# Optimization experiments

Measured on AMD Instinct MI355X. Metric: run time of the kernel, lower is better.

The kernel has to match this reference:

```python
import jax, jax.numpy as jnp
import numpy as np

VOCAB, DIM = 50257, 128
B, R, C, T = 8, 100, 100, 20


def setup_inputs() -> dict:
    key = jax.random.key(0)
    k1, k2, k3 = jax.random.split(key, 3)
    x = jax.random.randint(k1, (B, R, C, T), 0, VOCAB, dtype=jnp.int32)
    emb = jax.random.normal(k2, (VOCAB, DIM), dtype=jnp.float32)
    W = jax.random.normal(k3, (DIM, 1), dtype=jnp.float32) / np.sqrt(DIM)
    b = jnp.zeros((1,), dtype=jnp.float32)
    return {"x": x, "emb": emb, "W": W, "b": b}


def reference(x, emb, W, b):
    # x: [B,R,C,T] int ids -> gather: [B,R,C,T,D]
    e = emb[x]
    # aggregate = mean over tokens (dropout is identity in eval)
    agg = e.mean(axis=-2)                      # [B,R,C,D]
    h = jax.nn.gelu(agg, approximate=False)    # exact erf GELU (torch default)
    logits = jnp.einsum('brcd,do->brc', h, W) + b[0]
    return logits                              # [B,R,C]
```

## Files before the change

### kernel.cpp

```cpp
#include <hip/hip_runtime.h>
#include <hip/hip_bf16.h>
#include <math.h>

constexpr int T_TOK  = 20;
constexpr int DIM    = 128;
constexpr int VOCAB  = 50257;
constexpr int NSLICE = 4;
constexpr int SDIM   = DIM / NSLICE;

typedef unsigned int  uint32x4 __attribute__((ext_vector_type(4)));
typedef float         f32x2    __attribute__((ext_vector_type(2)));

__device__ __forceinline__ float erf_fast(float z) {
    const float az = fabsf(z);
    const float t  = __builtin_amdgcn_rcpf(fmaf(0.3275911f, az, 1.0f));
    float poly = fmaf(fmaf(fmaf(fmaf(1.061405429f, t, -1.453152027f),
                                t, 1.421413741f),
                           t, -0.284496736f),
                      t, 0.254829592f);
    poly *= t;
    const float e = __expf(-az * az);
    const float r = fmaf(-poly, e, 1.0f);
    return copysignf(r, z);
}

__global__ __launch_bounds__(256) void convert_kernel(
    const float* __restrict__ emb, const float* __restrict__ b,
    ushort* __restrict__ embt, float* __restrict__ out,
    int nb_emb, int n_out)
{
    if ((int)blockIdx.x < nb_emb) {
        const int i = blockIdx.x * 256 + threadIdx.x;
        if (i >= VOCAB * (DIM / 8)) return;
        const int v  = i >> 4;
        const int jc = i & 15;
        const int s  = jc >> 2;
        const int jj = jc & 3;

        const float* src = emb + (size_t)v * DIM + jc * 8;
        const float4 a = *reinterpret_cast<const float4*>(src);
        const float4 c = *reinterpret_cast<const float4*>(src + 4);

        auto pack2 = [](float lo, float hi) -> unsigned int {
            unsigned int l = __bfloat16_as_ushort(__float2bfloat16(lo));
            unsigned int h = __bfloat16_as_ushort(__float2bfloat16(hi));
            return l | (h << 16);
        };
        uint32x4 u = { pack2(a.x, a.y), pack2(a.z, a.w), pack2(c.x, c.y), pack2(c.z, c.w) };
        *reinterpret_cast<uint32x4*>(embt + ((size_t)s * VOCAB + v) * SDIM + jj * 8) = u;
    } else {
        const int i = ((int)blockIdx.x - nb_emb) * 256 + threadIdx.x;
        if (i < n_out) out[i] = b[0];
    }
}

__global__ __launch_bounds__(256) void gather_kernel(
    const int* __restrict__ x,
    const ushort* __restrict__ embt,
    const float* __restrict__ W,
    float* __restrict__ out,
    int n_out)
{
    const int s = blockIdx.x & (NSLICE - 1);
    const int o = ((int)blockIdx.x >> 2) * 32 + ((int)threadIdx.x >> 3);
    const int h = ((int)threadIdx.x >> 2) & 1;
    const int j = threadIdx.x & 3;
    if (o >= n_out) return;

    const int* xo = x + (size_t)o * T_TOK;
    int ids[10];
    {
        const int4 a = *reinterpret_cast<const int4*>(xo + (h ? 12 : 0));
        const int4 c = *reinterpret_cast<const int4*>(xo + (h ? 16 : 4));
        const int2 e = *reinterpret_cast<const int2*>(xo + (h ? 10 : 8));
        ids[0] = a.x; ids[1] = a.y; ids[2] = a.z; ids[3] = a.w;
        ids[4] = c.x; ids[5] = c.y; ids[6] = c.z; ids[7] = c.w;
        ids[8] = e.x; ids[9] = e.y;
    }

    const ushort* base = embt + (size_t)s * VOCAB * SDIM + j * 8;
    f32x2 acc[4] = {{0.f,0.f},{0.f,0.f},{0.f,0.f},{0.f,0.f}};

    #pragma unroll
    for (int t = 0; t < 10; ++t) {
        const uint32x4 u = *reinterpret_cast<const uint32x4*>(base + (size_t)ids[t] * SDIM);
        #pragma unroll
        for (int q = 0; q < 4; ++q) {
            f32x2 v = { __uint_as_float(u[q] << 16), __uint_as_float(u[q] & 0xffff0000u) };
            acc[q] += v;
        }
    }

    const float lo[4] = { acc[0].x, acc[0].y, acc[1].x, acc[1].y };
    const float hi[4] = { acc[2].x, acc[2].y, acc[3].x, acc[3].y };
    float sum[4];
    #pragma unroll
    for (int k = 0; k < 4; ++k) {
        const float send = (h == 0) ? hi[k] : lo[k];
        const float recv = __shfl_xor(send, 4, 64);
        const float keep = (h == 0) ? lo[k] : hi[k];
        sum[k] = keep + recv;
    }

    const float c_z = (1.0f / (float)T_TOK) * 0.70710678118654752440f;
    const float c_h = 0.5f / (float)T_TOK;
    const float* wp = W + s * SDIM + j * 8 + h * 4;
    float p = 0.f;
    #pragma unroll
    for (int k = 0; k < 4; ++k) {
        const float w  = wp[k];
        const float t1 = sum[k] * c_h * w;
        const float r  = erf_fast(sum[k] * c_z);
        p = fmaf(t1, r, p + t1);
    }

    p += __shfl_xor(p, 1, 64);
    p += __shfl_xor(p, 2, 64);
    p += __shfl_xor(p, 4, 64);

    if ((threadIdx.x & 7) == 0)
        __hip_atomic_fetch_add(out + o, p, __ATOMIC_RELAXED, __HIP_MEMORY_SCOPE_AGENT);
}

__global__ __launch_bounds__(256) void gelu_embed_fallback(
    const int* __restrict__ x, const float* __restrict__ emb,
    const float* __restrict__ W, const float* __restrict__ b,
    float* __restrict__ out, int n_out)
{
    const int wave = (int)((blockIdx.x * blockDim.x + threadIdx.x) >> 6);
    const int lane = (int)(threadIdx.x & 63);
    if (wave >= n_out) return;
    const int* ids = x + (size_t)wave * T_TOK;
    float2 acc = make_float2(0.f, 0.f);
    #pragma unroll
    for (int t = 0; t < T_TOK; ++t) {
        const int id = ids[t];
        const float2 v = *reinterpret_cast<const float2*>(
            emb + (size_t)id * DIM + (size_t)(lane * 2));
        acc.x += v.x; acc.y += v.y;
    }
    const float inv_t = 1.0f / (float)T_TOK;
    const float ax = acc.x * inv_t, ay = acc.y * inv_t;
    const float kInvSqrt2 = 0.70710678118654752440f;
    const float gx = 0.5f * ax * (1.0f + erff(ax * kInvSqrt2));
    const float gy = 0.5f * ay * (1.0f + erff(ay * kInvSqrt2));
    const float2 w = *reinterpret_cast<const float2*>(W + (size_t)(lane * 2));
    float p = gx * w.x + gy * w.y;
    #pragma unroll
    for (int off = 32; off >= 1; off >>= 1) p += __shfl_down(p, off, 64);
    if (lane == 0) out[wave] = p + b[0];
}

extern "C" void kernel_launch(void* const* d_in, const int* in_sizes, int n_in,
                              void* d_out, int out_size, void* d_ws, size_t ws_size,
                              hipStream_t stream) {
    const int*   x   = (const int*)d_in[0];
    const float* emb = (const float*)d_in[1];
    const float* W   = (const float*)d_in[2];
    const float* b   = (const float*)d_in[3];
    float* out = (float*)d_out;
    const int n_out = out_size;

    const size_t embt_bytes = (size_t)NSLICE * VOCAB * SDIM * sizeof(ushort);

    if (ws_size < embt_bytes) {
        const int blocks = (n_out + 3) / 4;
        gelu_embed_fallback<<<blocks, 256, 0, stream>>>(x, emb, W, b, out, n_out);
        return;
    }

    ushort* embt = (ushort*)d_ws;

    {
        const int nb_emb = (VOCAB * (DIM / 8) + 255) / 256;
        const int nb_out = (n_out + 255) / 256;
        convert_kernel<<<nb_emb + nb_out, 256, 0, stream>>>(emb, b, embt, out,
                                                            nb_emb, n_out);
    }
    {
        const int nchunk = (n_out + 31) / 32;
        gather_kernel<<<NSLICE * nchunk, 256, 0, stream>>>(x, embt, W, out, n_out);
    }
}
```

Baseline: 46.10 us.

## Assign embedding slices to blocks by XCC id via atomic work tickets

```diff
diff --git a/kernel.cpp b/kernel.cpp
--- a/kernel.cpp
+++ b/kernel.cpp
@@ -7,6 +7,7 @@
 constexpr int VOCAB  = 50257;
 constexpr int NSLICE = 4;
 constexpr int SDIM   = DIM / NSLICE;
+constexpr int OUTS_PER_BLOCK = 32;
 
 typedef unsigned int  uint32x4 __attribute__((ext_vector_type(4)));
 typedef float         f32x2    __attribute__((ext_vector_type(2)));
@@ -26,7 +27,7 @@
 
 __global__ __launch_bounds__(256) void convert_kernel(
     const float* __restrict__ emb, const float* __restrict__ b,
-    ushort* __restrict__ embt, float* __restrict__ out,
+    ushort* __restrict__ embt, float* __restrict__ out, int* __restrict__ ctr,
     int nb_emb, int n_out)
 {
     if ((int)blockIdx.x < nb_emb) {
@@ -51,6 +52,7 @@
     } else {
         const int i = ((int)blockIdx.x - nb_emb) * 256 + threadIdx.x;
         if (i < n_out) out[i] = b[0];
+        if (i < NSLICE) ctr[i] = 0;
     }
 }
 
@@ -59,10 +61,28 @@
     const ushort* __restrict__ embt,
     const float* __restrict__ W,
     float* __restrict__ out,
-    int n_out)
+    int* __restrict__ ctr,
+    int n_out, int nchunk)
 {
-    const int s = blockIdx.x & (NSLICE - 1);
-    const int o = ((int)blockIdx.x >> 2) * 32 + ((int)threadIdx.x >> 3);
+    __shared__ int s_ticket[2];
+    if (threadIdx.x == 0) {
+        const unsigned xcc = __builtin_amdgcn_s_getreg(((4 - 1) << 11) | 20);
+        const int pref = (int)(xcc & 3u);
+        int ss = -1, cc = -1;
+        for (int q = 0; q < NSLICE; ++q) {
+            const int s2 = (pref + q) & (NSLICE - 1);
+            const int t  = __hip_atomic_fetch_add(&ctr[s2], 1,
+                             __ATOMIC_RELAXED, __HIP_MEMORY_SCOPE_AGENT);
+            if (t < nchunk) { ss = s2; cc = t; break; }
+        }
+        s_ticket[0] = ss; s_ticket[1] = cc;
+    }
+    __syncthreads();
+    const int s = s_ticket[0];
+    const int c = s_ticket[1];
+    if (s < 0) return;
+
+    const int o = c * OUTS_PER_BLOCK + ((int)threadIdx.x >> 3);
     const int h = ((int)threadIdx.x >> 2) & 1;
     const int j = threadIdx.x & 3;
     if (o >= n_out) return;
@@ -71,10 +91,10 @@
     int ids[10];
     {
         const int4 a = *reinterpret_cast<const int4*>(xo + (h ? 12 : 0));
-        const int4 c = *reinterpret_cast<const int4*>(xo + (h ? 16 : 4));
+        const int4 cc4 = *reinterpret_cast<const int4*>(xo + (h ? 16 : 4));
         const int2 e = *reinterpret_cast<const int2*>(xo + (h ? 10 : 8));
         ids[0] = a.x; ids[1] = a.y; ids[2] = a.z; ids[3] = a.w;
-        ids[4] = c.x; ids[5] = c.y; ids[6] = c.z; ids[7] = c.w;
+        ids[4] = cc4.x; ids[5] = cc4.y; ids[6] = cc4.z; ids[7] = cc4.w;
         ids[8] = e.x; ids[9] = e.y;
     }
 
@@ -162,23 +182,27 @@
     const int n_out = out_size;
 
     const size_t embt_bytes = (size_t)NSLICE * VOCAB * SDIM * sizeof(ushort);
-
-    if (ws_size < embt_bytes) {
+    const size_t ctr_bytes  = 256;
+
+    if (ws_size < embt_bytes + ctr_bytes) {
         const int blocks = (n_out + 3) / 4;
         gelu_embed_fallback<<<blocks, 256, 0, stream>>>(x, emb, W, b, out, n_out);
         return;
     }
 
     ushort* embt = (ushort*)d_ws;
+    int*    ctr  = (int*)((char*)d_ws + embt_bytes);
+
+    const int nchunk = (n_out + OUTS_PER_BLOCK - 1) / OUTS_PER_BLOCK;
 
     {
         const int nb_emb = (VOCAB * (DIM / 8) + 255) / 256;
         const int nb_out = (n_out + 255) / 256;
-        convert_kernel<<<nb_emb + nb_out, 256, 0, stream>>>(emb, b, embt, out,
+        convert_kernel<<<nb_emb + nb_out, 256, 0, stream>>>(emb, b, embt, out, ctr,
                                                             nb_emb, n_out);
     }
     {
-        const int nchunk = (n_out + 31) / 32;
-        gather_kernel<<<NSLICE * nchunk, 256, 0, stream>>>(x, embt, W, out, n_out);
-    }
-}
+        gather_kernel<<<NSLICE * nchunk, 256, 0, stream>>>(x, embt, W, out, ctr,
+                                                           n_out, nchunk);
+    }
+}
```

After: 136.5 us. 196% more time.

## Quantize embedding table to int8 with per-row-slice scale packed in LSBs

Applied to the files above, without the earlier changes.

```diff
diff --git a/kernel.cpp b/kernel.cpp
--- a/kernel.cpp
+++ b/kernel.cpp
@@ -5,11 +5,10 @@
 constexpr int T_TOK  = 20;
 constexpr int DIM    = 128;
 constexpr int VOCAB  = 50257;
-constexpr int NSLICE = 4;
+constexpr int NSLICE = 2;
 constexpr int SDIM   = DIM / NSLICE;
 
-typedef unsigned int  uint32x4 __attribute__((ext_vector_type(4)));
-typedef float         f32x2    __attribute__((ext_vector_type(2)));
+typedef unsigned int uint32x4 __attribute__((ext_vector_type(4)));
 
 __device__ __forceinline__ float erf_fast(float z) {
     const float az = fabsf(z);
@@ -26,43 +25,63 @@
 
 __global__ __launch_bounds__(256) void convert_kernel(
     const float* __restrict__ emb, const float* __restrict__ b,
-    ushort* __restrict__ embt, float* __restrict__ out,
-    int nb_emb, int n_out)
+    unsigned char* __restrict__ embt8, float* __restrict__ out,
+    int nb_q, int n_out)
 {
-    if ((int)blockIdx.x < nb_emb) {
+    if ((int)blockIdx.x < nb_q) {
         const int i = blockIdx.x * 256 + threadIdx.x;
-        if (i >= VOCAB * (DIM / 8)) return;
-        const int v  = i >> 4;
-        const int jc = i & 15;
-        const int s  = jc >> 2;
-        const int jj = jc & 3;
-
-        const float* src = emb + (size_t)v * DIM + jc * 8;
-        const float4 a = *reinterpret_cast<const float4*>(src);
-        const float4 c = *reinterpret_cast<const float4*>(src + 4);
-
-        auto pack2 = [](float lo, float hi) -> unsigned int {
-            unsigned int l = __bfloat16_as_ushort(__float2bfloat16(lo));
-            unsigned int h = __bfloat16_as_ushort(__float2bfloat16(hi));
-            return l | (h << 16);
-        };
-        uint32x4 u = { pack2(a.x, a.y), pack2(a.z, a.w), pack2(c.x, c.y), pack2(c.z, c.w) };
-        *reinterpret_cast<uint32x4*>(embt + ((size_t)s * VOCAB + v) * SDIM + jj * 8) = u;
+        if (i >= VOCAB * NSLICE) return;
+        const int v = i >> 1;
+        const int s = i & 1;
+
+        const float* src = emb + (size_t)v * DIM + s * SDIM;
+        float vals[64];
+        float m = 0.f;
+        #pragma unroll
+        for (int q = 0; q < 16; ++q) {
+            const float4 f = *reinterpret_cast<const float4*>(src + q * 4);
+            vals[4*q+0] = f.x; vals[4*q+1] = f.y; vals[4*q+2] = f.z; vals[4*q+3] = f.w;
+            m = fmaxf(m, fmaxf(fmaxf(fabsf(f.x), fabsf(f.y)),
+                               fmaxf(fabsf(f.z), fabsf(f.w))));
+        }
+        int k = (int)ceilf((m - 1.78125f) * 4.0f);
+        k = max(0, min(15, k));
+        const float mhat = fmaf((float)k, 0.25f, 1.78125f);
+        const float inv  = 127.0f / mhat;
+
+        unsigned int w[16];
+        #pragma unroll
+        for (int q = 0; q < 16; ++q) {
+            const unsigned b0 = (unsigned)(__float2int_rn(vals[4*q+0] * inv) + 128);
+            const unsigned b1 = (unsigned)(__float2int_rn(vals[4*q+1] * inv) + 128);
+            const unsigned b2 = (unsigned)(__float2int_rn(vals[4*q+2] * inv) + 128);
+            const unsigned b3 = (unsigned)(__float2int_rn(vals[4*q+3] * inv) + 128);
+            w[q] = b0 | (b1 << 8) | (b2 << 16) | (b3 << 24);
+        }
+        const unsigned kk  = (unsigned)k;
+        const unsigned lsb = (kk & 1u) | ((kk & 2u) << 7) | ((kk & 4u) << 14) | ((kk & 8u) << 21);
+        w[0] = (w[0] & 0xFEFEFEFEu) | lsb;
+
+        uint32x4* dst = reinterpret_cast<uint32x4*>(embt8 + ((size_t)s * VOCAB + v) * 64);
+        dst[0] = uint32x4{ w[0],  w[1],  w[2],  w[3]  };
+        dst[1] = uint32x4{ w[4],  w[5],  w[6],  w[7]  };
+        dst[2] = uint32x4{ w[8],  w[9],  w[10], w[11] };
+        dst[3] = uint32x4{ w[12], w[13], w[14], w[15] };
     } else {
-        const int i = ((int)blockIdx.x - nb_emb) * 256 + threadIdx.x;
+        const int i = ((int)blockIdx.x - nb_q) * 256 + threadIdx.x;
         if (i < n_out) out[i] = b[0];
     }
 }
 
 __global__ __launch_bounds__(256) void gather_kernel(
     const int* __restrict__ x,
-    const ushort* __restrict__ embt,
+    const unsigned char* __restrict__ embt8,
     const float* __restrict__ W,
     float* __restrict__ out,
     int n_out)
 {
-    const int s = blockIdx.x & (NSLICE - 1);
-    const int o = ((int)blockIdx.x >> 2) * 32 + ((int)threadIdx.x >> 3);
+    const int s = blockIdx.x & 1;
+    const int o = ((int)blockIdx.x >> 1) * 32 + ((int)threadIdx.x >> 3);
     const int h = ((int)threadIdx.x >> 2) & 1;
     const int j = threadIdx.x & 3;
     if (o >= n_out) return;
@@ -78,39 +97,54 @@
         ids[8] = e.x; ids[9] = e.y;
     }
 
-    const ushort* base = embt + (size_t)s * VOCAB * SDIM + j * 8;
-    f32x2 acc[4] = {{0.f,0.f},{0.f,0.f},{0.f,0.f},{0.f,0.f}};
+    const unsigned char* base = embt8 + (size_t)s * VOCAB * 64 + j * 16;
+    const unsigned xmask = (j == 0) ? 0xFEFEFEFEu : 0xFFFFFFFFu;
+    const int blane = ((int)threadIdx.x & 63) & ~3;
+
+    float acc[16] = {0.f,0.f,0.f,0.f,0.f,0.f,0.f,0.f,
+                     0.f,0.f,0.f,0.f,0.f,0.f,0.f,0.f};
+    float ssum = 0.f;
 
     #pragma unroll
     for (int t = 0; t < 10; ++t) {
-        const uint32x4 u = *reinterpret_cast<const uint32x4*>(base + (size_t)ids[t] * SDIM);
+        uint32x4 u = *reinterpret_cast<const uint32x4*>(base + (size_t)ids[t] * 64);
+        const unsigned d0 = u.x;
+        const unsigned kb = (d0 & 1u) | ((d0 >> 7) & 2u) | ((d0 >> 14) & 4u) | ((d0 >> 21) & 8u);
+        float mh = fmaf((float)kb, 0.25f, 1.78125f);
+        mh = __shfl(mh, blane, 64);
+        ssum += mh;
+        u.x &= xmask;
         #pragma unroll
         for (int q = 0; q < 4; ++q) {
-            f32x2 v = { __uint_as_float(u[q] << 16), __uint_as_float(u[q] & 0xffff0000u) };
-            acc[q] += v;
+            const unsigned d = u[q];
+            acc[4*q+0] = fmaf(mh, (float)(d & 0xffu),         acc[4*q+0]);
+            acc[4*q+1] = fmaf(mh, (float)((d >> 8) & 0xffu),  acc[4*q+1]);
+            acc[4*q+2] = fmaf(mh, (float)((d >> 16) & 0xffu), acc[4*q+2]);
+            acc[4*q+3] = fmaf(mh, (float)(d >> 24),           acc[4*q+3]);
         }
     }
 
-    const float lo[4] = { acc[0].x, acc[0].y, acc[1].x, acc[1].y };
-    const float hi[4] = { acc[2].x, acc[2].y, acc[3].x, acc[3].y };
-    float sum[4];
-    #pragma unroll
-    for (int k = 0; k < 4; ++k) {
-        const float send = (h == 0) ? hi[k] : lo[k];
+    float sum[8];
+    #pragma unroll
+    for (int i = 0; i < 8; ++i) {
+        const float send = (h == 0) ? acc[8 + i] : acc[i];
         const float recv = __shfl_xor(send, 4, 64);
-        const float keep = (h == 0) ? lo[k] : hi[k];
-        sum[k] = keep + recv;
-    }
-
-    const float c_z = (1.0f / (float)T_TOK) * 0.70710678118654752440f;
-    const float c_h = 0.5f / (float)T_TOK;
-    const float* wp = W + s * SDIM + j * 8 + h * 4;
+        const float keep = (h == 0) ? acc[i] : acc[8 + i];
+        sum[i] = keep + recv;
+    }
+    const float S = ssum + __shfl_xor(ssum, 4, 64);
+
+    const float c_h = 0.5f / 2540.0f;
+    const float c_z = 0.70710678118654752440f / 2540.0f;
+    const float* wp = W + s * SDIM + j * 16 + h * 8;
     float p = 0.f;
     #pragma unroll
-    for (int k = 0; k < 4; ++k) {
-        const float w  = wp[k];
-        const float t1 = sum[k] * c_h * w;
-        const float r  = erf_fast(sum[k] * c_z);
+    for (int i = 0; i < 8; ++i) {
+        const float corr = (j == 0 && h == 0 && i < 4) ? 127.5f : 128.0f;
+        const float X  = fmaf(-corr, S, sum[i]);
+        const float w  = wp[i];
+        const float t1 = X * c_h * w;
+        const float r  = erf_fast(X * c_z);
         p = fmaf(t1, r, p + t1);
     }
 
@@ -161,7 +195,7 @@
     float* out = (float*)d_out;
     const int n_out = out_size;
 
-    const size_t embt_bytes = (size_t)NSLICE * VOCAB * SDIM * sizeof(ushort);
+    const size_t embt_bytes = (size_t)NSLICE * VOCAB * 64;
 
     if (ws_size < embt_bytes) {
         const int blocks = (n_out + 3) / 4;
@@ -169,16 +203,16 @@
         return;
     }
 
-    ushort* embt = (ushort*)d_ws;
+    unsigned char* embt8 = (unsigned char*)d_ws;
 
     {
-        const int nb_emb = (VOCAB * (DIM / 8) + 255) / 256;
+        const int nb_q   = (VOCAB * NSLICE + 255) / 256;
         const int nb_out = (n_out + 255) / 256;
-        convert_kernel<<<nb_emb + nb_out, 256, 0, stream>>>(emb, b, embt, out,
-                                                            nb_emb, n_out);
+        convert_kernel<<<nb_q + nb_out, 256, 0, stream>>>(emb, b, embt8, out,
+                                                          nb_q, n_out);
     }
     {
         const int nchunk = (n_out + 31) / 32;
-        gather_kernel<<<NSLICE * nchunk, 256, 0, stream>>>(x, embt, W, out, n_out);
-    }
-}
+        gather_kernel<<<NSLICE * nchunk, 256, 0, stream>>>(x, embt8, W, out, n_out);
+    }
+}
```

Result: faster. 39.44 us (-14.5%).
